# Kernel tuning notes

Measured on AMD Instinct MI355X. Metric: run time of the kernel, lower is better.

The kernel has to match this reference:

```python
import jax, jax.numpy as jnp
import numpy as np

P = 1024   # relation_size
H = 300    # hidden_size
E = 300    # embedding_size
V = 50000  # vocab size of tag_representation


def setup_inputs() -> dict:
    key = jax.random.key(0)
    k1, k2, k3, k4 = jax.random.split(key, 4)
    tag_rep = jax.random.normal(k1, (V, E), dtype=jnp.float32)
    # nn.Linear weight shape is [out_features, in_features] -> [H, E]; stacked over relations.
    Lp_w = jax.random.normal(k2, (P, H, E), dtype=jnp.float32) * 0.05
    Rp_w = jax.random.normal(k3, (P, H, E), dtype=jnp.float32) * 0.05
    relation = jax.random.randint(k4, (P,), 0, 2, dtype=jnp.int64)
    return {
        "tag_rep": tag_rep,
        "Lp_w": Lp_w,
        "Rp_w": Rp_w,
        "relation": relation,
        "tag1_idx": 7,
        "tag2_idx": 11,
    }


def reference(tag_rep, Lp_w, Rp_w, relation, tag1_idx, tag2_idx):
    wi = tag_rep[tag1_idx]  # [E]
    wj = tag_rep[tag2_idx]  # [E]
    # Batched per-relation projections: Linear(x) = W @ x for all P relations at once.
    li = jnp.einsum("phe,e->ph", Lp_w, wi)  # [P, H]
    rj = jnp.einsum("phe,e->ph", Rp_w, wj)  # [P, H]
    diff = li - rj                            # [P, H]
    # torch.norm(v, p=2)**2 over the whole vector == sum of squares.
    dist = jnp.sum(diff * diff, axis=-1)      # [P]
    is_edge = (relation == 1)
    is_not = (relation == 0)
    term1 = jnp.where(is_edge, dist, 0.0)
    term2 = jnp.where(is_not, dist, 0.0)
    n_edge = is_edge.astype(jnp.float32)
    not_edge = is_not.astype(jnp.float32)
    return jnp.stack([term1, term2, n_edge, not_edge])  # [4, P]
```

## Files before the change

kernel.cpp:

```cpp
#include <hip/hip_runtime.h>


#define KGE_P 1024
#define KGE_H 300
#define KGE_E 300
#define KGE_E4 75

__global__ __launch_bounds__(256) void kge_kernel(
    const float* __restrict__ tag_rep,
    const float* __restrict__ Lp_w,
    const float* __restrict__ Rp_w,
    const int*   __restrict__ relation,
    const int*   __restrict__ tag1_idx,
    const int*   __restrict__ tag2_idx,
    float*       __restrict__ out)
{
    __shared__ float s_wi[KGE_E];
    __shared__ float s_wj[KGE_E];
    __shared__ float s_wave[4];

    const int p    = blockIdx.x;
    const int tid  = threadIdx.x;
    const int lane = tid & 63;
    const int wave = tid >> 6;

    {
        const int t1 = tag1_idx[0];
        const int t2 = tag2_idx[0];
        const float* wi = tag_rep + (size_t)t1 * KGE_E;
        const float* wj = tag_rep + (size_t)t2 * KGE_E;
        for (int i = tid; i < KGE_E; i += 256) {
            s_wi[i] = wi[i];
            s_wj[i] = wj[i];
        }
    }
    __syncthreads();

    const float4* __restrict__ Lbase = (const float4*)(Lp_w + (size_t)p * KGE_H * KGE_E);
    const float4* __restrict__ Rbase = (const float4*)(Rp_w + (size_t)p * KGE_H * KGE_E);
    const float4* s_wi4 = (const float4*)s_wi;
    const float4* s_wj4 = (const float4*)s_wj;

    float dist_acc = 0.0f;

    for (int h = wave; h < KGE_H; h += 4) {
        const float4* __restrict__ Lr = Lbase + h * KGE_E4;
        const float4* __restrict__ Rr = Rbase + h * KGE_E4;

        float partial = 0.0f;
        for (int i = lane; i < KGE_E4; i += 64) {
            float4 lv = Lr[i];
            float4 rv = Rr[i];
            float4 a  = s_wi4[i];
            float4 b  = s_wj4[i];
            partial += lv.x * a.x + lv.y * a.y + lv.z * a.z + lv.w * a.w;
            partial -= rv.x * b.x + rv.y * b.y + rv.z * b.z + rv.w * b.w;
        }
        #pragma unroll
        for (int off = 32; off >= 1; off >>= 1)
            partial += __shfl_xor(partial, off, 64);

        dist_acc += partial * partial;
    }

    if (lane == 0) s_wave[wave] = dist_acc;
    __syncthreads();

    if (tid == 0) {
        const float dist = s_wave[0] + s_wave[1] + s_wave[2] + s_wave[3];
        const int rel = relation[p];
        const float is_edge = (rel == 1) ? 1.0f : 0.0f;
        const float is_not  = (rel == 0) ? 1.0f : 0.0f;
        out[0 * KGE_P + p] = dist * is_edge;
        out[1 * KGE_P + p] = dist * is_not;
        out[2 * KGE_P + p] = is_edge;
        out[3 * KGE_P + p] = is_not;
    }
}

extern "C" void kernel_launch(void* const* d_in, const int* in_sizes, int n_in,
                              void* d_out, int out_size, void* d_ws, size_t ws_size,
                              hipStream_t stream) {
    const float* tag_rep  = (const float*)d_in[0];
    const float* Lp_w     = (const float*)d_in[1];
    const float* Rp_w     = (const float*)d_in[2];
    const int*   relation = (const int*)d_in[3];
    const int*   tag1_idx = (const int*)d_in[4];
    const int*   tag2_idx = (const int*)d_in[5];
    float*       out      = (float*)d_out;

    kge_kernel<<<KGE_P, 256, 0, stream>>>(tag_rep, Lp_w, Rp_w,
                                          relation, tag1_idx, tag2_idx, out);
}
```

Measured before the change: 139.8 us.

## Split projection into 4x-parallel proj kernel plus separate distance reduction kernel

When workspace is large enough, the single fused kernel is replaced by two kernels. The first launches four blocks per relation, one per (matrix, half of H), and writes projected vectors to workspace. The second computes the squared distance per relation and writes the outputs. The aim is more blocks in flight to saturate memory bandwidth on the 2.5GB weight stream, at the cost of an extra launch and a workspace round trip; the fused fallback also hoists the shared-memory vectors into registers and unrolls the inner loop.

```diff
diff --git a/kernel.cpp b/kernel.cpp
--- a/kernel.cpp
+++ b/kernel.cpp
@@ -5,8 +5,93 @@
 #define KGE_H 300
 #define KGE_E 300
 #define KGE_E4 75
+#define KGE_TAILC 11
+#define KGE_HALF 150
 
-__global__ __launch_bounds__(256) void kge_kernel(
+__device__ __forceinline__ float dot4(float4 x, float4 y) {
+    return x.x * y.x + x.y * y.y + x.z * y.z + x.w * y.w;
+}
+
+__global__ __launch_bounds__(256) void kge_proj(
+    const float* __restrict__ tag_rep,
+    const float* __restrict__ Lp_w,
+    const float* __restrict__ Rp_w,
+    const int*   __restrict__ tag1_idx,
+    const int*   __restrict__ tag2_idx,
+    float*       __restrict__ ws)
+{
+    __shared__ float s_w[KGE_E];
+
+    const int b    = blockIdx.x;
+    const int p    = b >> 2;
+    const int m    = b & 1;
+    const int half = (b >> 1) & 1;
+    const int tid  = threadIdx.x;
+    const int lane = tid & 63;
+    const int wave = tid >> 6;
+
+    const int tag = (m == 0) ? tag1_idx[0] : tag2_idx[0];
+    const float* wrow = tag_rep + (size_t)tag * KGE_E;
+    for (int i = tid; i < KGE_E; i += 256) s_w[i] = wrow[i];
+    __syncthreads();
+
+    const float4* w4 = (const float4*)s_w;
+    const float4 a0 = w4[lane];
+    float4 a1 = make_float4(0.f, 0.f, 0.f, 0.f);
+    if (lane < KGE_TAILC) a1 = w4[64 + lane];
+
+    const float* mat = ((m == 0) ? Lp_w : Rp_w) + (size_t)p * KGE_H * KGE_E;
+    float* wsrow = ws + (size_t)(p * 2 + m) * KGE_H;
+
+    const int h0 = half * KGE_HALF;
+    const int h1 = h0 + KGE_HALF;
+    for (int h = h0 + wave; h < h1; h += 4) {
+        const float4* __restrict__ row = (const float4*)(mat + (size_t)h * KGE_E);
+        float4 v0 = row[lane];
+        float s = dot4(v0, a0);
+        if (lane < KGE_TAILC) {
+            float4 v1 = row[64 + lane];
+            s += dot4(v1, a1);
+        }
+        #pragma unroll
+        for (int off = 32; off >= 1; off >>= 1)
+            s += __shfl_xor(s, off, 64);
+        if (lane == 0) wsrow[h] = s;
+    }
+}
+
+__global__ __launch_bounds__(64) void kge_dist(
+    const float* __restrict__ ws,
+    const int*   __restrict__ relation,
+    float*       __restrict__ out)
+{
+    const int p    = blockIdx.x;
+    const int lane = threadIdx.x;
+
+    const float* li = ws + (size_t)(p * 2 + 0) * KGE_H;
+    const float* rj = ws + (size_t)(p * 2 + 1) * KGE_H;
+
+    float acc = 0.0f;
+    for (int h = lane; h < KGE_H; h += 64) {
+        float d = li[h] - rj[h];
+        acc += d * d;
+    }
+    #pragma unroll
+    for (int off = 32; off >= 1; off >>= 1)
+        acc += __shfl_xor(acc, off, 64);
+
+    if (lane == 0) {
+        const int rel = relation[p];
+        const float is_edge = (rel == 1) ? 1.0f : 0.0f;
+        const float is_not  = (rel == 0) ? 1.0f : 0.0f;
+        out[0 * KGE_P + p] = acc * is_edge;
+        out[1 * KGE_P + p] = acc * is_not;
+        out[2 * KGE_P + p] = is_edge;
+        out[3 * KGE_P + p] = is_not;
+    }
+}
+
+__global__ __launch_bounds__(256) void kge_fused(
     const float* __restrict__ tag_rep,
     const float* __restrict__ Lp_w,
     const float* __restrict__ Rp_w,
@@ -36,31 +121,36 @@
     }
     __syncthreads();
 
+    const float4* s_wi4 = (const float4*)s_wi;
+    const float4* s_wj4 = (const float4*)s_wj;
+    const float4 a0 = s_wi4[lane];
+    const float4 b0 = s_wj4[lane];
+    float4 a1 = make_float4(0.f, 0.f, 0.f, 0.f);
+    float4 b1 = a1;
+    if (lane < KGE_TAILC) {
+        a1 = s_wi4[64 + lane];
+        b1 = s_wj4[64 + lane];
+    }
+
     const float4* __restrict__ Lbase = (const float4*)(Lp_w + (size_t)p * KGE_H * KGE_E);
     const float4* __restrict__ Rbase = (const float4*)(Rp_w + (size_t)p * KGE_H * KGE_E);
-    const float4* s_wi4 = (const float4*)s_wi;
-    const float4* s_wj4 = (const float4*)s_wj;
 
     float dist_acc = 0.0f;
-
     for (int h = wave; h < KGE_H; h += 4) {
-        const float4* __restrict__ Lr = Lbase + h * KGE_E4;
-        const float4* __restrict__ Rr = Rbase + h * KGE_E4;
-
-        float partial = 0.0f;
-        for (int i = lane; i < KGE_E4; i += 64) {
-            float4 lv = Lr[i];
-            float4 rv = Rr[i];
-            float4 a  = s_wi4[i];
-            float4 b  = s_wj4[i];
-            partial += lv.x * a.x + lv.y * a.y + lv.z * a.z + lv.w * a.w;
-            partial -= rv.x * b.x + rv.y * b.y + rv.z * b.z + rv.w * b.w;
+        const float4* __restrict__ Lr = Lbase + (size_t)h * KGE_E4;
+        const float4* __restrict__ Rr = Rbase + (size_t)h * KGE_E4;
+        float4 lv = Lr[lane];
+        float4 rv = Rr[lane];
+        float s = dot4(lv, a0) - dot4(rv, b0);
+        if (lane < KGE_TAILC) {
+            float4 lb = Lr[64 + lane];
+            float4 rb = Rr[64 + lane];
+            s += dot4(lb, a1) - dot4(rb, b1);
         }
         #pragma unroll
         for (int off = 32; off >= 1; off >>= 1)
-            partial += __shfl_xor(partial, off, 64);
-
-        dist_acc += partial * partial;
+            s += __shfl_xor(s, off, 64);
+        dist_acc += s * s;
     }
 
     if (lane == 0) s_wave[wave] = dist_acc;
@@ -89,6 +179,14 @@
     const int*   tag2_idx = (const int*)d_in[5];
     float*       out      = (float*)d_out;
 
-    kge_kernel<<<KGE_P, 256, 0, stream>>>(tag_rep, Lp_w, Rp_w,
-                                          relation, tag1_idx, tag2_idx, out);
+    const size_t ws_needed = (size_t)2 * KGE_P * KGE_H * sizeof(float);
+    if (ws_size >= ws_needed) {
+        float* ws = (float*)d_ws;
+        kge_proj<<<4 * KGE_P, 256, 0, stream>>>(tag_rep, Lp_w, Rp_w,
+                                                tag1_idx, tag2_idx, ws);
+        kge_dist<<<KGE_P, 64, 0, stream>>>(ws, relation, out);
+    } else {
+        kge_fused<<<KGE_P, 256, 0, stream>>>(tag_rep, Lp_w, Rp_w,
+                                             relation, tag1_idx, tag2_idx, out);
+    }
 }
```

Result: slower. 158.3 us (+13.3%).
